# Kernel optimization log

Hardware: AMD Instinct MI355X
Metric: run time of the kernel (lower is better)

Reference implementation:

```python
import jax, jax.numpy as jnp
import numpy as np

EPS = 1e-10


def setup_inputs() -> dict:
    key = jax.random.key(0)
    kS, kQ, kW, kL = jax.random.split(key, 4)
    B, C, K, Q, D = 64, 20, 5, 15, 2048
    support = jax.random.normal(kS, (B * C * K, D), dtype=jnp.float32)
    query = jax.random.normal(kQ, (B * C * Q, D), dtype=jnp.float32)
    # encoder = single Linear(in_dim=D, hidden=D)
    W = jax.random.normal(kW, (D, D), dtype=jnp.float32) / np.sqrt(D)
    b = jnp.zeros((D,), dtype=jnp.float32)
    # one-hot support labels: each class appears K times per episode
    labels = jax.random.randint(kL, (B, C * K), 0, C)
    support_label_one_hot = jax.nn.one_hot(labels, C, dtype=jnp.float32)
    return {
        "support": support,
        "query": query,
        "support_label_one_hot": support_label_one_hot,
        "W": W,
        "b": b,
        "C": C,
        "K": K,
        "Q": Q,
    }


def reference(support, query, support_label_one_hot, W, b, C, K, Q):
    H = W.shape[1]
    # encoder (linear) on flat batches
    s = (support @ W + b).reshape(-1, C * K, H)   # [B, C*K, H]
    q = (query @ W + b).reshape(-1, C * Q, H)     # [B, C*Q, H]
    # DistanceNetwork: cosine-like similarity, only support magnitude normalized
    inv_norm = jax.lax.rsqrt(jnp.clip(jnp.sum(s * s, axis=-1), EPS, None))  # [B, C*K]
    sim = jnp.einsum("bqh,bsh->bqs", q, s) * inv_norm[:, None, :]           # [B, C*Q, C*K]
    # AttentionClassify: softmax over support set, then weighted sum of one-hot labels
    att = jax.nn.softmax(sim, axis=-1)                                       # [B, C*Q, C*K]
    preds = jnp.einsum("bqs,bsc->bqc", att, support_label_one_hot)          # [B, C*Q, C]
    probs = preds.reshape(-1, C)                                             # [B*C*Q, C]
    pred = jnp.argmax(probs, axis=1)
    return probs, pred
```

## Files before the change

### kernel.cpp

```cpp
#include <hip/hip_runtime.h>
#include <hip/hip_bf16.h>
#include <math.h>

#define BATCH 64
#define NCLS  20
#define NS    100
#define NQ    300
#define DIM   2048
#define MS    (BATCH * NS)
#define MQ    (BATCH * NQ)
#define KSPL  4
#define PROW  320
#define PCOL  112

typedef __attribute__((ext_vector_type(8))) short frag_ab;
typedef __attribute__((ext_vector_type(4))) float frag_cd;

union FAB { frag_ab f; unsigned u[4]; };

__device__ __forceinline__ unsigned rne_hi(float x) {
  unsigned u = __float_as_uint(x);
  return (u + 0x7FFFu + ((u >> 16) & 1u)) & 0xFFFF0000u;
}

__device__ __forceinline__ void split2rn(float x, float y, unsigned& p1,
                                         unsigned& p2) {
  union { __hip_bfloat162 h; unsigned u; } c1, c2;
  c1.h = __float22bfloat162_rn(make_float2(x, y));
  p1 = c1.u;
  float rx = x - __uint_as_float(c1.u << 16);
  float ry = y - __uint_as_float(c1.u & 0xFFFF0000u);
  c2.h = __float22bfloat162_rn(make_float2(rx, ry));
  p2 = c2.u;
}

#define GLL16(g, l)                                                            \
  __builtin_amdgcn_global_load_lds(                                            \
      (const __attribute__((address_space(1))) void*)(g),                      \
      (__attribute__((address_space(3))) void*)(l), 16, 0, 0)

__global__ __launch_bounds__(256) void esplit2(const float* __restrict__ X,
                                               unsigned short* __restrict__ X1,
                                               unsigned short* __restrict__ X2,
                                               int n4) {
  int i = blockIdx.x * 256 + threadIdx.x;
  if (i >= n4) return;
  float4 v = ((const float4*)X)[i];
  float x[4] = {v.x, v.y, v.z, v.w};
  ushort4 o1, o2;
  unsigned short* d1 = (unsigned short*)&o1;
  unsigned short* d2 = (unsigned short*)&o2;
#pragma unroll
  for (int q = 0; q < 4; ++q) {
    unsigned u1 = rne_hi(x[q]);
    float r1 = x[q] - __uint_as_float(u1);
    unsigned u2 = rne_hi(r1);
    d1[q] = (unsigned short)(u1 >> 16);
    d2[q] = (unsigned short)(u2 >> 16);
  }
  ((ushort4*)X1)[i] = o1;
  ((ushort4*)X2)[i] = o2;
}

template <int NH, int MINW, bool SPLIT>
__global__ __launch_bounds__(256, MINW) void gemm_mfma3(
    const float* __restrict__ X, const unsigned short* __restrict__ W1,
    const unsigned short* __restrict__ W2, const float* __restrict__ bias,
    float* __restrict__ Y, unsigned short* __restrict__ S1,
    unsigned short* __restrict__ S2) {
  __shared__ __align__(16) float          As[4][2][128][4];
  __shared__ __align__(16) unsigned short B1[4][128 * NH][8];
  __shared__ __align__(16) unsigned short B2[4][128 * NH][8];

  const int tid = threadIdx.x;
  const int w = tid >> 6, lane = tid & 63;
  const int ml = lane & 15, kq = lane >> 4;
  const int wm = (w >> 1) * 64, wn = (w & 1) * 64;
  const int col0 = blockIdx.x * (128 * NH), row0 = blockIdx.y * 128;

  frag_cd acc[NH][4][4];
#pragma unroll
  for (int h = 0; h < NH; ++h)
#pragma unroll
    for (int i = 0; i < 4; ++i)
#pragma unroll
      for (int j = 0; j < 4; ++j)
#pragma unroll
        for (int r = 0; r < 4; ++r) acc[h][i][j][r] = 0.f;

  for (int k0 = 0; k0 < DIM; k0 += 32) {
#pragma unroll
    for (int h = 0; h < 2; ++h)
#pragma unroll
      for (int mh = 0; mh < 2; ++mh) {
        const float* g =
            X + (size_t)(row0 + mh * 64 + lane) * DIM + k0 + w * 8 + h * 4;
        GLL16(g, &As[w][h][mh * 64][0]);
      }
#pragma unroll
    for (int t = 0; t < 2 * NH; ++t) {
      const size_t off = (size_t)(col0 + t * 64 + lane) * DIM + k0 + w * 8;
      GLL16(W1 + off, &B1[w][t * 64][0]);
      GLL16(W2 + off, &B2[w][t * 64][0]);
    }
    __syncthreads();

    FAB a1[4], a2[4];
#pragma unroll
    for (int i = 0; i < 4; ++i) {
      int m = wm + i * 16 + ml;
      float4 f0 = *(const float4*)&As[kq][0][m][0];
      float4 f1 = *(const float4*)&As[kq][1][m][0];
      split2rn(f0.x, f0.y, a1[i].u[0], a2[i].u[0]);
      split2rn(f0.z, f0.w, a1[i].u[1], a2[i].u[1]);
      split2rn(f1.x, f1.y, a1[i].u[2], a2[i].u[2]);
      split2rn(f1.z, f1.w, a1[i].u[3], a2[i].u[3]);
    }
#pragma unroll
    for (int nh = 0; nh < NH; ++nh) {
#pragma unroll
      for (int j = 0; j < 4; ++j) {
        int n = nh * 128 + wn + j * 16 + ml;
        FAB b1, b2;
        *(uint4*)&b1.u[0] = *(const uint4*)&B1[kq][n][0];
        *(uint4*)&b2.u[0] = *(const uint4*)&B2[kq][n][0];
#pragma unroll
        for (int i = 0; i < 4; ++i) {
          acc[nh][i][j] = __builtin_amdgcn_mfma_f32_16x16x32_bf16(
              a1[i].f, b1.f, acc[nh][i][j], 0, 0, 0);
          acc[nh][i][j] = __builtin_amdgcn_mfma_f32_16x16x32_bf16(
              a1[i].f, b2.f, acc[nh][i][j], 0, 0, 0);
          acc[nh][i][j] = __builtin_amdgcn_mfma_f32_16x16x32_bf16(
              a2[i].f, b1.f, acc[nh][i][j], 0, 0, 0);
        }
      }
    }
    __syncthreads();
  }

#pragma unroll
  for (int nh = 0; nh < NH; ++nh)
#pragma unroll
    for (int j = 0; j < 4; ++j) {
      int col = col0 + nh * 128 + wn + j * 16 + ml;
      float bv = bias ? bias[col] : 0.f;
#pragma unroll
      for (int i = 0; i < 4; ++i) {
        int rowb = row0 + wm + i * 16 + kq * 4;
#pragma unroll
        for (int r = 0; r < 4; ++r) {
          float val = acc[nh][i][j][r] + bv;
          size_t idx = (size_t)(rowb + r) * DIM + col;
          if (Y) Y[idx] = val;
          if (SPLIT) {
            unsigned u1 = rne_hi(val);
            float rr = val - __uint_as_float(u1);
            unsigned u2 = rne_hi(rr);
            S1[idx] = (unsigned short)(u1 >> 16);
            S2[idx] = (unsigned short)(u2 >> 16);
          }
        }
      }
    }
}

#define MFMA3(ACC, A1, A2, BV1, BV2)                                           \
  ACC = __builtin_amdgcn_mfma_f32_16x16x32_bf16(A1.f, BV1.f, ACC, 0, 0, 0);    \
  ACC = __builtin_amdgcn_mfma_f32_16x16x32_bf16(A1.f, BV2.f, ACC, 0, 0, 0);    \
  ACC = __builtin_amdgcn_mfma_f32_16x16x32_bf16(A2.f, BV1.f, ACC, 0, 0, 0)

#define SIMJ(J)                                                                \
  {                                                                            \
    FAB bf1, bf2;                                                              \
    *(uint4*)&bf1.u[0] = *(const uint4*)(z1b + o##J + k0);                     \
    *(uint4*)&bf2.u[0] = *(const uint4*)(z2b + o##J + k0);                     \
    MFMA3(acc##J, a1, a2, bf1, bf2);                                           \
  }

#define STJ(J)                                                                 \
  {                                                                            \
    const int n = J * 16 + ml;                                                 \
    part[pbase + 0 * PCOL + n] = acc##J[0];                                    \
    part[pbase + 1 * PCOL + n] = acc##J[1];                                    \
    part[pbase + 2 * PCOL + n] = acc##J[2];                                    \
    part[pbase + 3 * PCOL + n] = acc##J[3];                                    \
  }

__global__ __launch_bounds__(256) void sim2_part(
    const float* __restrict__ Xq, const unsigned short* __restrict__ Z1,
    const unsigned short* __restrict__ Z2, const float* __restrict__ wb,
    float* __restrict__ part, float* __restrict__ upart) {
  const int wg = blockIdx.x + 5 * blockIdx.y + 320 * blockIdx.z;
  const int swz = (wg & 7) * 160 + (wg >> 3);
  const int b = swz / 20;
  const int r20 = swz % 20;
  const int ks = r20 / 5;
  const int mt = r20 % 5;

  const int w = threadIdx.x >> 6, lane = threadIdx.x & 63;
  const int ml = lane & 15, kq = lane >> 4;

  int r = mt * 64 + w * 16 + ml;
  const int rc = r < NQ ? r : NQ - 1;
  const float* aptr = Xq + ((size_t)b * NQ + rc) * DIM + kq * 8;

  const unsigned short* z1b = Z1 + (size_t)b * NS * DIM + kq * 8;
  const unsigned short* z2b = Z2 + (size_t)b * NS * DIM + kq * 8;
  const int o0 = (0 * 16 + ml) * DIM;
  const int o1 = (1 * 16 + ml) * DIM;
  const int o2 = (2 * 16 + ml) * DIM;
  const int o3 = (3 * 16 + ml) * DIM;
  const int o4 = (4 * 16 + ml) * DIM;
  const int o5 = (5 * 16 + ml) * DIM;
  const int n6 = 6 * 16 + ml;
  const int o6 = (n6 < NS ? n6 : NS - 1) * DIM;

  frag_cd acc0 = {0.f, 0.f, 0.f, 0.f}, acc1 = {0.f, 0.f, 0.f, 0.f};
  frag_cd acc2 = {0.f, 0.f, 0.f, 0.f}, acc3 = {0.f, 0.f, 0.f, 0.f};
  frag_cd acc4 = {0.f, 0.f, 0.f, 0.f}, acc5 = {0.f, 0.f, 0.f, 0.f};
  frag_cd acc6 = {0.f, 0.f, 0.f, 0.f};
  float up = 0.f;

  const int kbeg = ks * (DIM / KSPL), kend = kbeg + DIM / KSPL;
#pragma unroll 2
  for (int k0 = kbeg; k0 < kend; k0 += 32) {
    float4 f0 = *(const float4*)(aptr + k0);
    float4 f1 = *(const float4*)(aptr + k0 + 4);
    float4 wa = *(const float4*)(wb + k0 + kq * 8);
    float4 wc = *(const float4*)(wb + k0 + kq * 8 + 4);
    up += f0.x * wa.x + f0.y * wa.y + f0.z * wa.z + f0.w * wa.w +
          f1.x * wc.x + f1.y * wc.y + f1.z * wc.z + f1.w * wc.w;
    FAB a1, a2;
    split2rn(f0.x, f0.y, a1.u[0], a2.u[0]);
    split2rn(f0.z, f0.w, a1.u[1], a2.u[1]);
    split2rn(f1.x, f1.y, a1.u[2], a2.u[2]);
    split2rn(f1.z, f1.w, a1.u[3], a2.u[3]);
    SIMJ(0); SIMJ(1); SIMJ(2); SIMJ(3); SIMJ(4); SIMJ(5); SIMJ(6);
  }

  up += __shfl_xor(up, 16, 64);
  up += __shfl_xor(up, 32, 64);
  if (lane < 16)
    upart[((size_t)ks * BATCH + b) * PROW + mt * 64 + w * 16 + ml] = up;

  const size_t pbase =
      (((size_t)ks * BATCH + b) * PROW + (mt * 64 + w * 16 + kq * 4)) * PCOL;
  STJ(0); STJ(1); STJ(2); STJ(3); STJ(4); STJ(5); STJ(6);
}

__global__ __launch_bounds__(256) void gemv_wb(const float* __restrict__ W,
                                               const float* __restrict__ b,
                                               float* __restrict__ wb,
                                               float* __restrict__ bb) {
  const int k = blockIdx.x;
  const int d0 = threadIdx.x * 8;
  float4 w0 = *(const float4*)(W + (size_t)k * DIM + d0);
  float4 w1 = *(const float4*)(W + (size_t)k * DIM + d0 + 4);
  float4 b0 = *(const float4*)(b + d0);
  float4 b1 = *(const float4*)(b + d0 + 4);
  float s = w0.x * b0.x + w0.y * b0.y + w0.z * b0.z + w0.w * b0.w +
            w1.x * b1.x + w1.y * b1.y + w1.z * b1.z + w1.w * b1.w;
#pragma unroll
  for (int off = 32; off; off >>= 1) s += __shfl_down(s, off, 64);
  __shared__ float red[4];
  if ((threadIdx.x & 63) == 0) red[threadIdx.x >> 6] = s;
  __syncthreads();
  if (threadIdx.x == 0) wb[k] = red[0] + red[1] + red[2] + red[3];
  if (k == 0) {
    float s2 = b0.x * b0.x + b0.y * b0.y + b0.z * b0.z + b0.w * b0.w +
               b1.x * b1.x + b1.y * b1.y + b1.z * b1.z + b1.w * b1.w;
#pragma unroll
    for (int off = 32; off; off >>= 1) s2 += __shfl_down(s2, off, 64);
    __syncthreads();
    if ((threadIdx.x & 63) == 0) red[threadIdx.x >> 6] = s2;
    __syncthreads();
    if (threadIdx.x == 0) bb[0] = red[0] + red[1] + red[2] + red[3];
  }
}

__global__ __launch_bounds__(256) void norm_v(const float* __restrict__ Z,
                                              const float* __restrict__ Xs,
                                              const float* __restrict__ wb,
                                              const float* __restrict__ bb,
                                              float* __restrict__ inv_norm,
                                              float* __restrict__ vv) {
  const int row = blockIdx.x;
  const int d0 = threadIdx.x * 8;
  const float* zp = Z + (size_t)row * DIM + d0;
  const float* xp = Xs + (size_t)row * DIM + d0;
  float4 z0 = *(const float4*)zp, z1 = *(const float4*)(zp + 4);
  float4 x0 = *(const float4*)xp, x1 = *(const float4*)(xp + 4);
  float4 w0 = *(const float4*)(wb + d0), w1 = *(const float4*)(wb + d0 + 4);
  float s1 = z0.x * x0.x + z0.y * x0.y + z0.z * x0.z + z0.w * x0.w +
             z1.x * x1.x + z1.y * x1.y + z1.z * x1.z + z1.w * x1.w;
  float s2 = x0.x * w0.x + x0.y * w0.y + x0.z * w0.z + x0.w * w0.w +
             x1.x * w1.x + x1.y * w1.y + x1.z * w1.z + x1.w * w1.w;
#pragma unroll
  for (int off = 32; off; off >>= 1) {
    s1 += __shfl_down(s1, off, 64);
    s2 += __shfl_down(s2, off, 64);
  }
  __shared__ float r1[4], r2[4];
  if ((threadIdx.x & 63) == 0) {
    r1[threadIdx.x >> 6] = s1;
    r2[threadIdx.x >> 6] = s2;
  }
  __syncthreads();
  if (threadIdx.x == 0) {
    float t1 = r1[0] + r1[1] + r1[2] + r1[3];
    float t2 = r2[0] + r2[1] + r2[2] + r2[3];
    float nn = t1 + 2.f * t2 + bb[0];
    inv_norm[row] = rsqrtf(fmaxf(nn, 1e-10f));
    vv[row] = t2;
  }
}

__global__ __launch_bounds__(256) void softmax_part(
    const float* __restrict__ part, const float* __restrict__ upart,
    const float* __restrict__ vv, const float* __restrict__ bb,
    const float* __restrict__ inv_norm, const float* __restrict__ onehot,
    float* __restrict__ out) {
  const int wave = threadIdx.x >> 6;
  const int lane = threadIdx.x & 63;
  const int r = blockIdx.x * 4 + wave;
  const int b = r / NQ;
  const int m = r - b * NQ;
  const size_t kstr = (size_t)BATCH * PROW * PCOL;
  const size_t ustr = (size_t)BATCH * PROW;
  const float* p0 = part + ((size_t)b * PROW + m) * PCOL;
  const float* up0 = upart + (size_t)b * PROW + m;
  const float bbv = bb[0];
  const float ur = up0[0] + up0[ustr] + up0[2 * ustr] + up0[3 * ustr];

  float raw1 = p0[lane] + p0[kstr + lane] + p0[2 * kstr + lane] +
               p0[3 * kstr + lane];
  float v1 = (raw1 + ur + vv[b * NS + lane] + bbv) * inv_norm[b * NS + lane];
  float v2 = -INFINITY;
  if (lane < NS - 64) {
    const int n = lane + 64;
    float raw2 = p0[n] + p0[kstr + n] + p0[2 * kstr + n] + p0[3 * kstr + n];
    v2 = (raw2 + ur + vv[b * NS + n] + bbv) * inv_norm[b * NS + n];
  }
  float mx = fmaxf(v1, v2);
#pragma unroll
  for (int off = 32; off; off >>= 1) mx = fmaxf(mx, __shfl_xor(mx, off, 64));
  float e1 = expf(v1 - mx);
  float e2 = (lane < NS - 64) ? expf(v2 - mx) : 0.f;
  float ssum = e1 + e2;
#pragma unroll
  for (int off = 32; off; off >>= 1) ssum += __shfl_xor(ssum, off, 64);
  float inv = 1.0f / ssum;
  __shared__ float att[4][NS];
  __shared__ float pr[4][NCLS];
  att[wave][lane] = e1 * inv;
  if (lane < NS - 64) att[wave][lane + 64] = e2 * inv;
  __syncthreads();
  if (lane < NCLS) {
    const float* oh = onehot + ((size_t)b * NS) * NCLS + lane;
    float p = 0.f;
#pragma unroll 4
    for (int j = 0; j < NS; ++j) p += att[wave][j] * oh[(size_t)j * NCLS];
    out[(size_t)r * NCLS + lane] = p;
    pr[wave][lane] = p;
  }
  __syncthreads();
  if (lane == 0) {
    int best = 0;
    float bv = pr[wave][0];
    for (int c = 1; c < NCLS; ++c) {
      float v = pr[wave][c];
      if (v > bv) { bv = v; best = c; }
    }
    out[(size_t)MQ * NCLS + r] = (float)best;
  }
}

__global__ __launch_bounds__(256) void softmax_fb(
    const float* __restrict__ sim, const float* __restrict__ onehot,
    float* __restrict__ out) {
  const int wave = threadIdx.x >> 6;
  const int lane = threadIdx.x & 63;
  const int r = blockIdx.x * 4 + wave;
  const int b = r / NQ;
  const float* srow = sim + (size_t)r * NS;
  float v1 = srow[lane];
  float v2 = (lane < NS - 64) ? srow[lane + 64] : -INFINITY;
  float m = fmaxf(v1, v2);
#pragma unroll
  for (int off = 32; off; off >>= 1) m = fmaxf(m, __shfl_xor(m, off, 64));
  float e1 = expf(v1 - m);
  float e2 = (lane < NS - 64) ? expf(v2 - m) : 0.f;
  float ssum = e1 + e2;
#pragma unroll
  for (int off = 32; off; off >>= 1) ssum += __shfl_xor(ssum, off, 64);
  float inv = 1.0f / ssum;
  __shared__ float att[4][NS];
  __shared__ float pr[4][NCLS];
  att[wave][lane] = e1 * inv;
  if (lane < NS - 64) att[wave][lane + 64] = e2 * inv;
  __syncthreads();
  if (lane < NCLS) {
    const float* oh = onehot + ((size_t)b * NS) * NCLS + lane;
    float p = 0.f;
#pragma unroll 4
    for (int j = 0; j < NS; ++j) p += att[wave][j] * oh[(size_t)j * NCLS];
    out[(size_t)r * NCLS + lane] = p;
    pr[wave][lane] = p;
  }
  __syncthreads();
  if (lane == 0) {
    int best = 0;
    float bv = pr[wave][0];
    for (int c = 1; c < NCLS; ++c) {
      float v = pr[wave][c];
      if (v > bv) { bv = v; best = c; }
    }
    out[(size_t)MQ * NCLS + r] = (float)best;
  }
}

__global__ __launch_bounds__(256) void gemm_xw(const float* __restrict__ X,
                                               const float* __restrict__ W,
                                               const float* __restrict__ bias,
                                               float* __restrict__ Y) {
  __shared__ float As[16][64];
  __shared__ float Bs[16][64];
  const int t = threadIdx.x;
  const int row0 = blockIdx.x * 64;
  const int col0 = blockIdx.y * 64;
  const int am = t >> 2, ak = (t & 3) * 4;
  const int bk = t >> 4, bn = (t & 15) * 4;
  const int tm = (t >> 4) * 4, tn = (t & 15) * 4;
  float acc[4][4] = {};
  for (int k0 = 0; k0 < DIM; k0 += 16) {
    float4 av = *(const float4*)(X + (size_t)(row0 + am) * DIM + k0 + ak);
    As[ak + 0][am] = av.x;
    As[ak + 1][am] = av.y;
    As[ak + 2][am] = av.z;
    As[ak + 3][am] = av.w;
    *(float4*)&Bs[bk][bn] =
        *(const float4*)(W + (size_t)(k0 + bk) * DIM + col0 + bn);
    __syncthreads();
#pragma unroll
    for (int k = 0; k < 16; ++k) {
      float4 a4 = *(const float4*)&As[k][tm];
      float4 b4 = *(const float4*)&Bs[k][tn];
      float av_[4] = {a4.x, a4.y, a4.z, a4.w};
      float bv_[4] = {b4.x, b4.y, b4.z, b4.w};
#pragma unroll
      for (int i = 0; i < 4; ++i)
#pragma unroll
        for (int j = 0; j < 4; ++j) acc[i][j] += av_[i] * bv_[j];
    }
    __syncthreads();
  }
  float4 bbv = *(const float4*)(bias + col0 + tn);
  float bv_[4] = {bbv.x, bbv.y, bbv.z, bbv.w};
#pragma unroll
  for (int i = 0; i < 4; ++i) {
    float4 o;
    o.x = acc[i][0] + bv_[0];
    o.y = acc[i][1] + bv_[1];
    o.z = acc[i][2] + bv_[2];
    o.w = acc[i][3] + bv_[3];
    *(float4*)(Y + (size_t)(row0 + tm + i) * DIM + col0 + tn) = o;
  }
}

__global__ __launch_bounds__(256) void norm_kernel(const float* __restrict__ s,
                                                   float* __restrict__ inv_norm) {
  const int row = blockIdx.x;
  const float* p = s + (size_t)row * DIM;
  const int d0 = threadIdx.x * 8;
  float4 a = *(const float4*)(p + d0);
  float4 b = *(const float4*)(p + d0 + 4);
  float sum = a.x * a.x + a.y * a.y + a.z * a.z + a.w * a.w +
              b.x * b.x + b.y * b.y + b.z * b.z + b.w * b.w;
#pragma unroll
  for (int off = 32; off; off >>= 1) sum += __shfl_down(sum, off, 64);
  __shared__ float red[4];
  if ((threadIdx.x & 63) == 0) red[threadIdx.x >> 6] = sum;
  __syncthreads();
  if (threadIdx.x == 0) {
    float tot = red[0] + red[1] + red[2] + red[3];
    inv_norm[row] = rsqrtf(fmaxf(tot, 1e-10f));
  }
}

__global__ __launch_bounds__(256) void sim_kernel(const float* __restrict__ q,
                                                  const float* __restrict__ s,
                                                  const float* __restrict__ inv_norm,
                                                  float* __restrict__ sim) {
  __shared__ float As[16][64];
  __shared__ float Bs[16][64];
  const int t = threadIdx.x;
  const int b = blockIdx.z;
  const int row0 = blockIdx.y * 64;
  const int col0 = blockIdx.x * 64;
  const float* qb = q + (size_t)b * NQ * DIM;
  const float* sb = s + (size_t)b * NS * DIM;
  const int am = t >> 2, ak = (t & 3) * 4;
  const int tm = (t >> 4) * 4, tn = (t & 15) * 4;
  float acc[4][4] = {};
  for (int k0 = 0; k0 < DIM; k0 += 16) {
    float4 av = make_float4(0.f, 0.f, 0.f, 0.f);
    if (row0 + am < NQ)
      av = *(const float4*)(qb + (size_t)(row0 + am) * DIM + k0 + ak);
    As[ak + 0][am] = av.x;
    As[ak + 1][am] = av.y;
    As[ak + 2][am] = av.z;
    As[ak + 3][am] = av.w;
    float4 bv = make_float4(0.f, 0.f, 0.f, 0.f);
    if (col0 + am < NS)
      bv = *(const float4*)(sb + (size_t)(col0 + am) * DIM + k0 + ak);
    Bs[ak + 0][am] = bv.x;
    Bs[ak + 1][am] = bv.y;
    Bs[ak + 2][am] = bv.z;
    Bs[ak + 3][am] = bv.w;
    __syncthreads();
#pragma unroll
    for (int k = 0; k < 16; ++k) {
      float4 a4 = *(const float4*)&As[k][tm];
      float4 b4 = *(const float4*)&Bs[k][tn];
      float av_[4] = {a4.x, a4.y, a4.z, a4.w};
      float bv_[4] = {b4.x, b4.y, b4.z, b4.w};
#pragma unroll
      for (int i = 0; i < 4; ++i)
#pragma unroll
        for (int j = 0; j < 4; ++j) acc[i][j] += av_[i] * bv_[j];
    }
    __syncthreads();
  }
#pragma unroll
  for (int i = 0; i < 4; ++i) {
    int m = row0 + tm + i;
    if (m >= NQ) continue;
#pragma unroll
    for (int j = 0; j < 4; ++j) {
      int n = col0 + tn + j;
      if (n >= NS) continue;
      sim[((size_t)b * NQ + m) * NS + n] = acc[i][j] * inv_norm[b * NS + n];
    }
  }
}

extern "C" void kernel_launch(void* const* d_in, const int* in_sizes, int n_in,
                              void* d_out, int out_size, void* d_ws,
                              size_t ws_size, hipStream_t stream) {
  const float* support = (const float*)d_in[0];
  const float* query   = (const float*)d_in[1];
  const float* onehot  = (const float*)d_in[2];
  const float* W       = (const float*)d_in[3];
  const float* bias    = (const float*)d_in[4];

  char* wsb = (char*)d_ws;

  const size_t NEED = 163333376;

  if (ws_size >= NEED) {
    float* Z              = (float*)wsb;
    unsigned short* Wr1   = (unsigned short*)(wsb + (size_t)69206016);
    unsigned short* Wr2   = (unsigned short*)(wsb + (size_t)77594624);
    unsigned short* G1    = (unsigned short*)(wsb + (size_t)85983232);
    unsigned short* G2    = (unsigned short*)(wsb + (size_t)94371840);
    unsigned short* Z1    = (unsigned short*)(wsb + (size_t)102760448);
    unsigned short* Z2    = (unsigned short*)(wsb + (size_t)128974848);
    float* part           = (float*)(wsb + (size_t)52428800);
    float* inv_norm       = (float*)(wsb + (size_t)162869248);
    float* vv             = (float*)(wsb + (size_t)162894848);
    float* wb             = (float*)(wsb + (size_t)162997248);
    float* bb             = (float*)(wsb + (size_t)163005440);
    float* upart          = (float*)(wsb + (size_t)163005696);

    esplit2<<<DIM * DIM / 1024, 256, 0, stream>>>(W, Wr1, Wr2, DIM * DIM / 4);
    gemm_mfma3<1, 3, true><<<dim3(DIM / 128, DIM / 128), 256, 0, stream>>>(
        W, Wr1, Wr2, nullptr, nullptr, G1, G2);
    gemm_mfma3<1, 3, true><<<dim3(DIM / 128, MS / 128), 256, 0, stream>>>(
        support, G1, G2, nullptr, Z, Z1, Z2);
    gemv_wb<<<DIM, 256, 0, stream>>>(W, bias, wb, bb);
    norm_v<<<MS, 256, 0, stream>>>(Z, support, wb, bb, inv_norm, vv);
    sim2_part<<<dim3(5, BATCH, KSPL), 256, 0, stream>>>(query, Z1, Z2, wb,
                                                        part, upart);
    softmax_part<<<MQ / 4, 256, 0, stream>>>(part, upart, vv, bb, inv_norm,
                                             onehot, (float*)d_out);
  } else {
    float* s = (float*)wsb;
    float* q = (float*)(wsb + (size_t)52428800);
    float* inv_norm = q + (size_t)MQ * DIM;
    float* sim      = inv_norm + MS;
    gemm_xw<<<dim3(MS / 64, DIM / 64), 256, 0, stream>>>(support, W, bias, s);
    gemm_xw<<<dim3(MQ / 64, DIM / 64), 256, 0, stream>>>(query, W, bias, q);
    norm_kernel<<<MS, 256, 0, stream>>>(s, inv_norm);
    sim_kernel<<<dim3(2, 5, BATCH), 256, 0, stream>>>(q, s, inv_norm, sim);
    softmax_fb<<<MQ / 4, 256, 0, stream>>>(sim, onehot, (float*)d_out);
  }
}
```

Baseline: 902.9 us.

## Pre-split GEMM A operands to bf16 pairs and widen support GEMM tile

Adds an esplit2 pass over the support matrix and rewrites the GEMM kernel to take pre-split bf16 hi/lo A operands from memory instead of loading fp32 and splitting in the inner loop. The W·W product reuses the already split W. The support GEMM switches to NH=2, a 128x256 tile, and both GEMMs drop to a minimum occupancy of 2 waves. This removes repeated per-tile split ALU work and halves fp32 A traffic per k-step. In exchange it adds an extra kernel pass that writes and reads about 52MB of split support data and needs a larger workspace.

```diff
diff --git a/kernel.cpp b/kernel.cpp
--- a/kernel.cpp
+++ b/kernel.cpp
@@ -62,15 +62,16 @@
   ((ushort4*)X2)[i] = o2;
 }
 
-template <int NH, int MINW, bool SPLIT>
-__global__ __launch_bounds__(256, MINW) void gemm_mfma3(
-    const float* __restrict__ X, const unsigned short* __restrict__ W1,
-    const unsigned short* __restrict__ W2, const float* __restrict__ bias,
-    float* __restrict__ Y, unsigned short* __restrict__ S1,
-    unsigned short* __restrict__ S2) {
-  __shared__ __align__(16) float          As[4][2][128][4];
-  __shared__ __align__(16) unsigned short B1[4][128 * NH][8];
-  __shared__ __align__(16) unsigned short B2[4][128 * NH][8];
+template <int NH, int MINW>
+__global__ __launch_bounds__(256, MINW) void gemm_bb3(
+    const unsigned short* __restrict__ A1, const unsigned short* __restrict__ A2,
+    const unsigned short* __restrict__ B1, const unsigned short* __restrict__ B2,
+    float* __restrict__ Y, unsigned short* __restrict__ S1o,
+    unsigned short* __restrict__ S2o) {
+  __shared__ __align__(16) unsigned short A1s[4][128][8];
+  __shared__ __align__(16) unsigned short A2s[4][128][8];
+  __shared__ __align__(16) unsigned short B1s[4][128 * NH][8];
+  __shared__ __align__(16) unsigned short B2s[4][128 * NH][8];
 
   const int tid = threadIdx.x;
   const int w = tid >> 6, lane = tid & 63;
@@ -90,18 +91,16 @@
 
   for (int k0 = 0; k0 < DIM; k0 += 32) {
 #pragma unroll
-    for (int h = 0; h < 2; ++h)
-#pragma unroll
-      for (int mh = 0; mh < 2; ++mh) {
-        const float* g =
-            X + (size_t)(row0 + mh * 64 + lane) * DIM + k0 + w * 8 + h * 4;
-        GLL16(g, &As[w][h][mh * 64][0]);
-      }
+    for (int mh = 0; mh < 2; ++mh) {
+      const size_t off = (size_t)(row0 + mh * 64 + lane) * DIM + k0 + w * 8;
+      GLL16(A1 + off, &A1s[w][mh * 64][0]);
+      GLL16(A2 + off, &A2s[w][mh * 64][0]);
+    }
 #pragma unroll
     for (int t = 0; t < 2 * NH; ++t) {
       const size_t off = (size_t)(col0 + t * 64 + lane) * DIM + k0 + w * 8;
-      GLL16(W1 + off, &B1[w][t * 64][0]);
-      GLL16(W2 + off, &B2[w][t * 64][0]);
+      GLL16(B1 + off, &B1s[w][t * 64][0]);
+      GLL16(B2 + off, &B2s[w][t * 64][0]);
     }
     __syncthreads();
 
@@ -109,12 +108,8 @@
 #pragma unroll
     for (int i = 0; i < 4; ++i) {
       int m = wm + i * 16 + ml;
-      float4 f0 = *(const float4*)&As[kq][0][m][0];
-      float4 f1 = *(const float4*)&As[kq][1][m][0];
-      split2rn(f0.x, f0.y, a1[i].u[0], a2[i].u[0]);
-      split2rn(f0.z, f0.w, a1[i].u[1], a2[i].u[1]);
-      split2rn(f1.x, f1.y, a1[i].u[2], a2[i].u[2]);
-      split2rn(f1.z, f1.w, a1[i].u[3], a2[i].u[3]);
+      *(uint4*)&a1[i].u[0] = *(const uint4*)&A1s[kq][m][0];
+      *(uint4*)&a2[i].u[0] = *(const uint4*)&A2s[kq][m][0];
     }
 #pragma unroll
     for (int nh = 0; nh < NH; ++nh) {
@@ -122,8 +117,8 @@
       for (int j = 0; j < 4; ++j) {
         int n = nh * 128 + wn + j * 16 + ml;
         FAB b1, b2;
-        *(uint4*)&b1.u[0] = *(const uint4*)&B1[kq][n][0];
-        *(uint4*)&b2.u[0] = *(const uint4*)&B2[kq][n][0];
+        *(uint4*)&b1.u[0] = *(const uint4*)&B1s[kq][n][0];
+        *(uint4*)&b2.u[0] = *(const uint4*)&B2s[kq][n][0];
 #pragma unroll
         for (int i = 0; i < 4; ++i) {
           acc[nh][i][j] = __builtin_amdgcn_mfma_f32_16x16x32_bf16(
@@ -143,22 +138,19 @@
 #pragma unroll
     for (int j = 0; j < 4; ++j) {
       int col = col0 + nh * 128 + wn + j * 16 + ml;
-      float bv = bias ? bias[col] : 0.f;
 #pragma unroll
       for (int i = 0; i < 4; ++i) {
         int rowb = row0 + wm + i * 16 + kq * 4;
 #pragma unroll
         for (int r = 0; r < 4; ++r) {
-          float val = acc[nh][i][j][r] + bv;
+          float val = acc[nh][i][j][r];
           size_t idx = (size_t)(rowb + r) * DIM + col;
           if (Y) Y[idx] = val;
-          if (SPLIT) {
-            unsigned u1 = rne_hi(val);
-            float rr = val - __uint_as_float(u1);
-            unsigned u2 = rne_hi(rr);
-            S1[idx] = (unsigned short)(u1 >> 16);
-            S2[idx] = (unsigned short)(u2 >> 16);
-          }
+          unsigned u1 = rne_hi(val);
+          float rr = val - __uint_as_float(u1);
+          unsigned u2 = rne_hi(rr);
+          S1o[idx] = (unsigned short)(u1 >> 16);
+          S2o[idx] = (unsigned short)(u2 >> 16);
         }
       }
     }
@@ -555,28 +547,32 @@
 
   char* wsb = (char*)d_ws;
 
-  const size_t NEED = 163333376;
+  const size_t NEED = 191228160;
 
   if (ws_size >= NEED) {
     float* Z              = (float*)wsb;
-    unsigned short* Wr1   = (unsigned short*)(wsb + (size_t)69206016);
-    unsigned short* Wr2   = (unsigned short*)(wsb + (size_t)77594624);
-    unsigned short* G1    = (unsigned short*)(wsb + (size_t)85983232);
-    unsigned short* G2    = (unsigned short*)(wsb + (size_t)94371840);
-    unsigned short* Z1    = (unsigned short*)(wsb + (size_t)102760448);
-    unsigned short* Z2    = (unsigned short*)(wsb + (size_t)128974848);
+    unsigned short* S1    = (unsigned short*)(wsb + (size_t)52428800);
+    unsigned short* S2    = (unsigned short*)(wsb + (size_t)78643200);
+    unsigned short* Wr1   = (unsigned short*)(wsb + (size_t)104857600);
+    unsigned short* Wr2   = (unsigned short*)(wsb + (size_t)113246208);
+    unsigned short* G1    = (unsigned short*)(wsb + (size_t)121634816);
+    unsigned short* G2    = (unsigned short*)(wsb + (size_t)130023424);
+    unsigned short* Z1    = (unsigned short*)(wsb + (size_t)138412032);
+    unsigned short* Z2    = (unsigned short*)(wsb + (size_t)164626432);
     float* part           = (float*)(wsb + (size_t)52428800);
-    float* inv_norm       = (float*)(wsb + (size_t)162869248);
-    float* vv             = (float*)(wsb + (size_t)162894848);
-    float* wb             = (float*)(wsb + (size_t)162997248);
-    float* bb             = (float*)(wsb + (size_t)163005440);
-    float* upart          = (float*)(wsb + (size_t)163005696);
+    float* inv_norm       = (float*)(wsb + (size_t)190840832);
+    float* vv             = (float*)(wsb + (size_t)190866432);
+    float* wb             = (float*)(wsb + (size_t)190892032);
+    float* bb             = (float*)(wsb + (size_t)190900224);
+    float* upart          = (float*)(wsb + (size_t)190900480);
 
     esplit2<<<DIM * DIM / 1024, 256, 0, stream>>>(W, Wr1, Wr2, DIM * DIM / 4);
-    gemm_mfma3<1, 3, true><<<dim3(DIM / 128, DIM / 128), 256, 0, stream>>>(
-        W, Wr1, Wr2, nullptr, nullptr, G1, G2);
-    gemm_mfma3<1, 3, true><<<dim3(DIM / 128, MS / 128), 256, 0, stream>>>(
-        support, G1, G2, nullptr, Z, Z1, Z2);
+    esplit2<<<MS * DIM / 1024, 256, 0, stream>>>(support, S1, S2,
+                                                 MS * DIM / 4);
+    gemm_bb3<1, 2><<<dim3(DIM / 128, DIM / 128), 256, 0, stream>>>(
+        Wr1, Wr2, Wr1, Wr2, nullptr, G1, G2);
+    gemm_bb3<2, 2><<<dim3(DIM / 256, MS / 128), 256, 0, stream>>>(
+        S1, S2, G1, G2, Z, Z1, Z2);
     gemv_wb<<<DIM, 256, 0, stream>>>(W, bias, wb, bb);
     norm_v<<<MS, 256, 0, stream>>>(Z, support, wb, bb, inv_norm, vv);
     sim2_part<<<dim3(5, BATCH, KSPL), 256, 0, stream>>>(query, Z1, Z2, wb,
```

Result: faster. 747.8 us (-17.2%).
